# Kernel tuning notes

Hardware: AMD Instinct MI355X
Metric: run time of the kernel (lower is better)

## Reference

```python
import jax, jax.numpy as jnp
import numpy as np

INPUT_DIMS = (8, 16, 8)
OUTPUT_DIMS = (8, 16, 8)
TT_RANKS = (1, 8, 8, 1)
SUP = 4
OUT_DIM = int(np.prod(OUTPUT_DIMS))


def _glorot(key, shape):
    # GlorotUniform over full core shape (matches keras initializer semantics closely enough
    # for a correctness baseline; exact init values are not part of the math being tested)
    fan_in = shape[0] * shape[1]
    fan_out = shape[2] * shape[3]
    limit = (6.0 / (fan_in + fan_out)) ** 0.5
    return jax.random.uniform(key, shape, jnp.float32, -limit, limit)


def setup_inputs() -> dict:
    key = jax.random.key(0)
    kx, k0, k1, k2 = jax.random.split(key, 4)
    x = jax.random.normal(kx, (2, 2048, 1024), dtype=jnp.float32)
    core0 = _glorot(k0, (TT_RANKS[0], INPUT_DIMS[0], OUTPUT_DIMS[0], TT_RANKS[1], SUP))
    core1 = _glorot(k1, (TT_RANKS[1], INPUT_DIMS[1], OUTPUT_DIMS[1], TT_RANKS[2], SUP))
    core2 = _glorot(k2, (TT_RANKS[2], INPUT_DIMS[2], OUTPUT_DIMS[2], TT_RANKS[3], SUP))
    return {"x": x, "core0": core0, "core1": core1, "core2": core2}


def reference(x, core0, core1, core2):
    B, S, _ = x.shape
    n = B * S
    # [n, i0, i1, i2]
    res = x.reshape(n, *INPUT_DIMS)
    # core0 has leading TT-rank 1 -> squeeze: (i0, o0, r1, s)
    c0 = core0[0]
    # contract input mode 0: n i0 i1 i2 , i0 o0 r1 s -> n o0 i1 i2 r1 s
    res = jnp.einsum('nbcd,bwqs->nwcdqs', res, c0)
    # contract input mode 1 + rank r1: -> n o0 o1 i2 r2 s
    res = jnp.einsum('nwcdqs,qcxrs->nwxdrs', res, core1)
    # contract input mode 2 + rank r2: -> n o0 o1 o2 r3 s  (r3 == 1)
    res = jnp.einsum('nwxdrs,rdyts->nwxyts', res, core2)
    res = jnp.squeeze(res, axis=-2)  # drop trailing rank-1 axis
    out = res.reshape(n, OUT_DIM, SUP)
    return out.reshape(B, S, OUT_DIM, SUP)
```

## Files before the change

### kernel.cpp

```cpp
#include <hip/hip_runtime.h>
#include <stdint.h>

typedef unsigned short u16;
typedef unsigned int u32;
typedef __bf16 bf16x8 __attribute__((ext_vector_type(8)));
typedef float f32x4 __attribute__((ext_vector_type(4)));

#define MFMA16 __builtin_amdgcn_mfma_f32_16x16x32_bf16


__device__ __forceinline__ u16 f2bf(float f) {
    u32 u = __builtin_bit_cast(u32, f);
    u32 r = (u + 0x7FFFu + ((u >> 16) & 1u)) >> 16;
    return (u16)r;
}

__device__ __forceinline__ void gload_lds16(const u16* g, u16* l) {
    __builtin_amdgcn_global_load_lds(
        (const __attribute__((address_space(1))) void*)g,
        (__attribute__((address_space(3))) void*)l,
        16, 0, 0);
}


__global__ __launch_bounds__(256) void pre_kernel(const float* __restrict__ x,
                                                  const float* __restrict__ c0,
                                                  const float* __restrict__ c1,
                                                  const float* __restrict__ c2,
                                                  u16* __restrict__ xb,
                                                  u16* __restrict__ Wt,
                                                  int convBlocks, int nElem) {
    __shared__ float smem[10496];
    const int t = threadIdx.x;

    if ((int)blockIdx.x < convBlocks) {
        int i = (blockIdx.x * 256 + t) * 8;
        if (i + 8 > nElem) return;
        float4 a = *reinterpret_cast<const float4*>(x + i);
        float4 b = *reinterpret_cast<const float4*>(x + i + 4);
        uint4 pk;
        pk.x = (u32)f2bf(a.x) | ((u32)f2bf(a.y) << 16);
        pk.y = (u32)f2bf(a.z) | ((u32)f2bf(a.w) << 16);
        pk.z = (u32)f2bf(b.x) | ((u32)f2bf(b.y) << 16);
        pk.w = (u32)f2bf(b.z) | ((u32)f2bf(b.w) << 16);
        *reinterpret_cast<uint4*>(xb + i) = pk;
        return;
    }

    float* l_c0 = smem;
    float* l_c1 = smem + 256;
    float* l_c2 = smem + 4352;
    float* l_w1 = smem + 6400;

    const int bid = blockIdx.x - convBlocks;
    const int bc = bid >> 2;
    const int part = bid & 3;
    const int b = bc >> 4, c = bc & 15;

    l_c0[t] = c0[b * 256 + t];
#pragma unroll
    for (int q = 0; q < 8; ++q) {
        l_c1[q * 512 + t]       = c1[(q * 16 + c) * 512 + t];
        l_c1[q * 512 + t + 256] = c1[(q * 16 + c) * 512 + t + 256];
    }
#pragma unroll
    for (int j = 0; j < 8; ++j) l_c2[t + 256 * j] = c2[t + 256 * j];
    __syncthreads();

#pragma unroll
    for (int j = 0; j < 4; ++j) {
        int idx = t + 256 * (part * 4 + j);
        int s = idx & 3;
        int r = (idx >> 2) & 7;
        int xx = (idx >> 5) & 15;
        int w = idx >> 9;
        float acc = 0.f;
#pragma unroll
        for (int q = 0; q < 8; ++q)
            acc += l_c0[(w * 8 + q) * 4 + s] * l_c1[q * 512 + (xx * 8 + r) * 4 + s];
        l_w1[idx] = acc;
    }
    __syncthreads();

#pragma unroll
    for (int j = 0; j < 4; ++j) {
        int idx = t + 256 * (part * 4 + j);
        int s = idx & 3;
        int y = (idx >> 2) & 7;
        int xx = (idx >> 5) & 15;
        int w = idx >> 9;
        float acc[8] = {0.f, 0.f, 0.f, 0.f, 0.f, 0.f, 0.f, 0.f};
#pragma unroll
        for (int r = 0; r < 8; ++r) {
            float w1 = l_w1[((w * 16 + xx) * 8 + r) * 4 + s];
#pragma unroll
            for (int d = 0; d < 8; ++d)
                acc[d] += w1 * l_c2[((r * 8 + d) * 8 + y) * 4 + s];
        }
        uint4 pk;
        pk.x = (u32)f2bf(acc[0]) | ((u32)f2bf(acc[1]) << 16);
        pk.y = (u32)f2bf(acc[2]) | ((u32)f2bf(acc[3]) << 16);
        pk.z = (u32)f2bf(acc[4]) | ((u32)f2bf(acc[5]) << 16);
        pk.w = (u32)f2bf(acc[6]) | ((u32)f2bf(acc[7]) << 16);
        *reinterpret_cast<uint4*>(&Wt[(size_t)idx * 1024 + b * 128 + c * 8]) = pk;
    }
}


#define SLOT_U16 16384

#define BAR() __builtin_amdgcn_s_barrier()

__global__ __launch_bounds__(512, 2) void gemm256_kernel(const u16* __restrict__ A,
                                                         const u16* __restrict__ B,
                                                         float* __restrict__ C,
                                                         int M, int N, int K) {
    __shared__ u16 As[2 * SLOT_U16];
    __shared__ u16 Bs[2 * SLOT_U16];

    const int t   = threadIdx.x;
    const int ln  = t & 63;
    const int wid = t >> 6;
    const int wr  = wid >> 2;
    const int wc  = wid & 3;

    const int bid = blockIdx.x;
    const int xcd = bid & 7;
    const int r8  = bid >> 3;
    const int bx  = (xcd & 1) * 8 + (r8 & 7);
    const int by  = (xcd >> 1) * 4 + (r8 >> 3);
    const int m0  = by * 256;
    const int n0  = bx * 256;
    const int NT  = K >> 6;

    const int frow  = ln & 15;
    const int koff0 = (((ln >> 4)    ) ^ (ln & 7)) * 8;
    const int koff1 = (((ln >> 4) + 4) ^ (ln & 7)) * 8;
    const int arow0 = (wr * 128 + frow) * 64;
    const int brow0 = (wc * 64  + frow) * 64;

    const int srow = t >> 3;
    const int scol = ((t & 7) ^ (srow & 7)) * 8;
    const u16* Asrc = A + (size_t)(m0 + srow) * K + scol;
    const u16* Bsrc = B + (size_t)(n0 + srow) * K + scol;

    f32x4 acc[8][4] = {};

#define STG(SRC, DST, H, L, KC)                                              \
    gload_lds16(SRC + (size_t)((H) * 128 + (L) * 64) * K + (KC),             \
                DST + (H) * 8192 + (L) * 4096 + t * 8);

#define READ_A(PH)                                                           \
    a0k0 = *(const bf16x8*)(Ab + arow0 + (2 * (PH)) * 1024 + koff0);         \
    a0k1 = *(const bf16x8*)(Ab + arow0 + (2 * (PH)) * 1024 + koff1);         \
    a1k0 = *(const bf16x8*)(Ab + arow0 + (2 * (PH) + 1) * 1024 + koff0);     \
    a1k1 = *(const bf16x8*)(Ab + arow0 + (2 * (PH) + 1) * 1024 + koff1);

#define MFMA_PH(PH)                                                          \
    _Pragma("unroll")                                                        \
    for (int n = 0; n < 4; ++n) {                                            \
        acc[2*(PH)][n]   = MFMA16(a0k0, bf[n][0], acc[2*(PH)][n],   0,0,0);  \
        acc[2*(PH)][n]   = MFMA16(a0k1, bf[n][1], acc[2*(PH)][n],   0,0,0);  \
        acc[2*(PH)+1][n] = MFMA16(a1k0, bf[n][0], acc[2*(PH)+1][n], 0,0,0);  \
        acc[2*(PH)+1][n] = MFMA16(a1k1, bf[n][1], acc[2*(PH)+1][n], 0,0,0);  \
    }

    STG(Bsrc, Bs, 0, 0, 0) STG(Bsrc, Bs, 0, 1, 0)
    STG(Bsrc, Bs, 1, 0, 0) STG(Bsrc, Bs, 1, 1, 0)
    STG(Asrc, As, 0, 0, 0) STG(Asrc, As, 1, 0, 0)
    STG(Asrc, As, 0, 1, 0) STG(Asrc, As, 1, 1, 0)
    asm volatile("s_waitcnt vmcnt(0)" ::: "memory");
    BAR();

    for (int kt = 0; kt < NT; ++kt) {
        const u16* Ab = As + (kt & 1) * SLOT_U16;
        const u16* Bb = Bs + (kt & 1) * SLOT_U16;
        u16* An = As + ((kt + 1) & 1) * SLOT_U16;
        u16* Bn = Bs + ((kt + 1) & 1) * SLOT_U16;
        const bool pf = (kt + 1) < NT;
        const int kc = (kt + 1) * 64;

        bf16x8 bf[4][2];
        bf16x8 a0k0, a0k1, a1k0, a1k1;

#pragma unroll
        for (int n = 0; n < 4; ++n) {
            bf[n][0] = *(const bf16x8*)(Bb + brow0 + n * 1024 + koff0);
            bf[n][1] = *(const bf16x8*)(Bb + brow0 + n * 1024 + koff1);
        }
        READ_A(0)
        if (pf) { STG(Bsrc, Bn, 0, 0, kc) STG(Bsrc, Bn, 0, 1, kc) }
        BAR();
        __builtin_amdgcn_s_setprio(1);
        MFMA_PH(0)
        __builtin_amdgcn_s_setprio(0);
        BAR();

        READ_A(1)
        if (pf) { STG(Bsrc, Bn, 1, 0, kc) STG(Bsrc, Bn, 1, 1, kc) }
        BAR();
        __builtin_amdgcn_s_setprio(1);
        MFMA_PH(1)
        __builtin_amdgcn_s_setprio(0);
        if (pf) { asm volatile("s_waitcnt vmcnt(4)" ::: "memory"); }
        else    { asm volatile("s_waitcnt vmcnt(0)" ::: "memory"); }
        BAR();

        READ_A(2)
        if (pf) { STG(Asrc, An, 0, 0, kc) STG(Asrc, An, 1, 0, kc) }
        BAR();
        __builtin_amdgcn_s_setprio(1);
        MFMA_PH(2)
        __builtin_amdgcn_s_setprio(0);
        BAR();

        READ_A(3)
        if (pf) { STG(Asrc, An, 0, 1, kc) STG(Asrc, An, 1, 1, kc) }
        BAR();
        __builtin_amdgcn_s_setprio(1);
        MFMA_PH(3)
        __builtin_amdgcn_s_setprio(0);
        if (pf) { asm volatile("s_waitcnt vmcnt(2)" ::: "memory"); }
        BAR();
    }
#undef MFMA_PH
#undef READ_A
#undef STG

    const int cr = (ln >> 4) * 4;
    const int cc = ln & 15;
#pragma unroll
    for (int fm = 0; fm < 8; ++fm) {
#pragma unroll
        for (int rr = 0; rr < 4; ++rr) {
            int row = m0 + wr * 128 + fm * 16 + cr + rr;
            float* p = C + (size_t)row * N + n0 + wc * 64 + cc;
#pragma unroll
            for (int fn = 0; fn < 4; ++fn)
                p[fn * 16] = acc[fm][fn][rr];
        }
    }
}


extern "C" void kernel_launch(void* const* d_in, const int* in_sizes, int n_in,
                              void* d_out, int out_size, void* d_ws, size_t ws_size,
                              hipStream_t stream) {
    const float* x  = (const float*)d_in[0];
    const float* c0 = (const float*)d_in[1];
    const float* c1 = (const float*)d_in[2];
    const float* c2 = (const float*)d_in[3];
    float* out = (float*)d_out;

    const int K = 1024;
    const int N = 4096;
    const int M = in_sizes[0] / K;

    u16* xb = (u16*)d_ws;
    u16* Wt = (u16*)d_ws + (size_t)M * K;

    const int convBlocks = (M * K) / (256 * 8);
    pre_kernel<<<convBlocks + 512, 256, 0, stream>>>(x, c0, c1, c2, xb, Wt,
                                                     convBlocks, M * K);

    gemm256_kernel<<<(N / 256) * (M / 256), 512, 0, stream>>>(xb, Wt, out, M, N, K);
}
```

Measured before the change: 58.19 us.

## Fuse fp32-to-bf16 conversion of x into GEMM A-tile staging

The separate pass that converted x to bf16 in workspace is removed. The GEMM now reads fp32 x directly through registers, converts it, and writes it into LDS, so the bf16 copy of x is no longer written and read back. The pipeline is also restructured: all B prefetches are issued at the start of each k-step, the fine-grained barriers and setprio phases are dropped, and one __syncthreads per iteration remains. In exchange the GEMM reads twice as many A bytes, uses more registers for staging, and relies on the compiler to place waits instead of explicit vmcnt control.

```diff
diff --git a/kernel.cpp b/kernel.cpp
--- a/kernel.cpp
+++ b/kernel.cpp
@@ -23,36 +23,19 @@
 }
 
 
-__global__ __launch_bounds__(256) void pre_kernel(const float* __restrict__ x,
-                                                  const float* __restrict__ c0,
-                                                  const float* __restrict__ c1,
-                                                  const float* __restrict__ c2,
-                                                  u16* __restrict__ xb,
-                                                  u16* __restrict__ Wt,
-                                                  int convBlocks, int nElem) {
+__global__ __launch_bounds__(256) void prep_w_kernel(const float* __restrict__ c0,
+                                                     const float* __restrict__ c1,
+                                                     const float* __restrict__ c2,
+                                                     u16* __restrict__ Wt) {
     __shared__ float smem[10496];
     const int t = threadIdx.x;
-
-    if ((int)blockIdx.x < convBlocks) {
-        int i = (blockIdx.x * 256 + t) * 8;
-        if (i + 8 > nElem) return;
-        float4 a = *reinterpret_cast<const float4*>(x + i);
-        float4 b = *reinterpret_cast<const float4*>(x + i + 4);
-        uint4 pk;
-        pk.x = (u32)f2bf(a.x) | ((u32)f2bf(a.y) << 16);
-        pk.y = (u32)f2bf(a.z) | ((u32)f2bf(a.w) << 16);
-        pk.z = (u32)f2bf(b.x) | ((u32)f2bf(b.y) << 16);
-        pk.w = (u32)f2bf(b.z) | ((u32)f2bf(b.w) << 16);
-        *reinterpret_cast<uint4*>(xb + i) = pk;
-        return;
-    }
 
     float* l_c0 = smem;
     float* l_c1 = smem + 256;
     float* l_c2 = smem + 4352;
     float* l_w1 = smem + 6400;
 
-    const int bid = blockIdx.x - convBlocks;
+    const int bid = blockIdx.x;
     const int bc = bid >> 2;
     const int part = bid & 3;
     const int b = bc >> 4, c = bc & 15;
@@ -109,9 +92,7 @@
 
 #define SLOT_U16 16384
 
-#define BAR() __builtin_amdgcn_s_barrier()
-
-__global__ __launch_bounds__(512, 2) void gemm256_kernel(const u16* __restrict__ A,
+__global__ __launch_bounds__(512, 2) void gemm256_kernel(const float* __restrict__ X,
                                                          const u16* __restrict__ B,
                                                          float* __restrict__ C,
                                                          int M, int N, int K) {
@@ -141,14 +122,28 @@
 
     const int srow = t >> 3;
     const int scol = ((t & 7) ^ (srow & 7)) * 8;
-    const u16* Asrc = A + (size_t)(m0 + srow) * K + scol;
     const u16* Bsrc = B + (size_t)(n0 + srow) * K + scol;
 
+    const float* Xsrc = X + (size_t)(m0 + srow) * K + scol;
+    const int awst = srow * 64 + (t & 7) * 8;
+
     f32x4 acc[8][4] = {};
 
-#define STG(SRC, DST, H, L, KC)                                              \
-    gload_lds16(SRC + (size_t)((H) * 128 + (L) * 64) * K + (KC),             \
-                DST + (H) * 8192 + (L) * 4096 + t * 8);
+#define STG_B(H, L, KC, DST)                                                 \
+    gload_lds16(Bsrc + (size_t)((H) * 128 + (L) * 64) * K + (KC),            \
+                (DST) + (H) * 8192 + (L) * 4096 + t * 8);
+
+#define A_LOAD(J, KC)                                                        \
+    av##J##a = *reinterpret_cast<const float4*>(Xsrc + (size_t)(64 * (J)) * K + (KC)); \
+    av##J##b = *reinterpret_cast<const float4*>(Xsrc + (size_t)(64 * (J)) * K + (KC) + 4);
+
+#define A_WRITE(J, DST)                                                      \
+    {   bf16x8 pk;                                                           \
+        pk[0] = (__bf16)av##J##a.x; pk[1] = (__bf16)av##J##a.y;              \
+        pk[2] = (__bf16)av##J##a.z; pk[3] = (__bf16)av##J##a.w;              \
+        pk[4] = (__bf16)av##J##b.x; pk[5] = (__bf16)av##J##b.y;              \
+        pk[6] = (__bf16)av##J##b.z; pk[7] = (__bf16)av##J##b.w;              \
+        *reinterpret_cast<bf16x8*>((DST) + awst + 4096 * (J)) = pk;   }
 
 #define READ_A(PH)                                                           \
     a0k0 = *(const bf16x8*)(Ab + arow0 + (2 * (PH)) * 1024 + koff0);         \
@@ -165,12 +160,12 @@
         acc[2*(PH)+1][n] = MFMA16(a1k1, bf[n][1], acc[2*(PH)+1][n], 0,0,0);  \
     }
 
-    STG(Bsrc, Bs, 0, 0, 0) STG(Bsrc, Bs, 0, 1, 0)
-    STG(Bsrc, Bs, 1, 0, 0) STG(Bsrc, Bs, 1, 1, 0)
-    STG(Asrc, As, 0, 0, 0) STG(Asrc, As, 1, 0, 0)
-    STG(Asrc, As, 0, 1, 0) STG(Asrc, As, 1, 1, 0)
-    asm volatile("s_waitcnt vmcnt(0)" ::: "memory");
-    BAR();
+    float4 av0a, av0b, av1a, av1b, av2a, av2b, av3a, av3b;
+
+    STG_B(0, 0, 0, Bs) STG_B(0, 1, 0, Bs) STG_B(1, 0, 0, Bs) STG_B(1, 1, 0, Bs)
+    A_LOAD(0, 0) A_LOAD(1, 0) A_LOAD(2, 0) A_LOAD(3, 0)
+    A_WRITE(0, As) A_WRITE(1, As) A_WRITE(2, As) A_WRITE(3, As)
+    __syncthreads();
 
     for (int kt = 0; kt < NT; ++kt) {
         const u16* Ab = As + (kt & 1) * SLOT_U16;
@@ -183,49 +178,40 @@
         bf16x8 bf[4][2];
         bf16x8 a0k0, a0k1, a1k0, a1k1;
 
+        if (pf) {
+            STG_B(0, 0, kc, Bn) STG_B(0, 1, kc, Bn)
+            STG_B(1, 0, kc, Bn) STG_B(1, 1, kc, Bn)
+            A_LOAD(0, kc) A_LOAD(1, kc)
+        }
+
 #pragma unroll
         for (int n = 0; n < 4; ++n) {
             bf[n][0] = *(const bf16x8*)(Bb + brow0 + n * 1024 + koff0);
             bf[n][1] = *(const bf16x8*)(Bb + brow0 + n * 1024 + koff1);
         }
         READ_A(0)
-        if (pf) { STG(Bsrc, Bn, 0, 0, kc) STG(Bsrc, Bn, 0, 1, kc) }
-        BAR();
-        __builtin_amdgcn_s_setprio(1);
         MFMA_PH(0)
-        __builtin_amdgcn_s_setprio(0);
-        BAR();
-
         READ_A(1)
-        if (pf) { STG(Bsrc, Bn, 1, 0, kc) STG(Bsrc, Bn, 1, 1, kc) }
-        BAR();
-        __builtin_amdgcn_s_setprio(1);
         MFMA_PH(1)
-        __builtin_amdgcn_s_setprio(0);
-        if (pf) { asm volatile("s_waitcnt vmcnt(4)" ::: "memory"); }
-        else    { asm volatile("s_waitcnt vmcnt(0)" ::: "memory"); }
-        BAR();
+
+        if (pf) {
+            A_WRITE(0, An) A_WRITE(1, An)
+            A_LOAD(2, kc) A_LOAD(3, kc)
+        }
 
         READ_A(2)
-        if (pf) { STG(Asrc, An, 0, 0, kc) STG(Asrc, An, 1, 0, kc) }
-        BAR();
-        __builtin_amdgcn_s_setprio(1);
         MFMA_PH(2)
-        __builtin_amdgcn_s_setprio(0);
-        BAR();
-
         READ_A(3)
-        if (pf) { STG(Asrc, An, 0, 1, kc) STG(Asrc, An, 1, 1, kc) }
-        BAR();
-        __builtin_amdgcn_s_setprio(1);
         MFMA_PH(3)
-        __builtin_amdgcn_s_setprio(0);
-        if (pf) { asm volatile("s_waitcnt vmcnt(2)" ::: "memory"); }
-        BAR();
+
+        if (pf) { A_WRITE(2, An) A_WRITE(3, An) }
+        __syncthreads();
     }
 #undef MFMA_PH
 #undef READ_A
-#undef STG
+#undef A_WRITE
+#undef A_LOAD
+#undef STG_B
 
     const int cr = (ln >> 4) * 4;
     const int cc = ln & 15;
@@ -256,12 +242,8 @@
     const int N = 4096;
     const int M = in_sizes[0] / K;
 
-    u16* xb = (u16*)d_ws;
-    u16* Wt = (u16*)d_ws + (size_t)M * K;
-
-    const int convBlocks = (M * K) / (256 * 8);
-    pre_kernel<<<convBlocks + 512, 256, 0, stream>>>(x, c0, c1, c2, xb, Wt,
-                                                     convBlocks, M * K);
-
-    gemm256_kernel<<<(N / 256) * (M / 256), 512, 0, stream>>>(xb, Wt, out, M, N, K);
-}
+    u16* Wt = (u16*)d_ws;
+
+    prep_w_kernel<<<512, 256, 0, stream>>>(c0, c1, c2, Wt);
+    gemm256_kernel<<<(N / 256) * (M / 256), 512, 0, stream>>>(x, Wt, out, M, N, K);
+}
```

New measurement: 58.99 us. Within noise of the previous version (+1.4%).
